# Optimization experiments

Hardware: AMD Instinct MI355X
Metric: run time of the kernel (lower is better)

Reference implementation:

```python
import jax, jax.numpy as jnp
import numpy as np

EPS = 1e-08
NUM_EMBEDDINGS = 8192
EMBEDDING_DIM = 256
N_TOKENS = 32768


def setup_inputs() -> dict:
    key = jax.random.key(0)
    k1, k2, k3 = jax.random.split(key, 3)
    input_data = jax.random.normal(k1, (N_TOKENS, EMBEDDING_DIM), dtype=jnp.float32)
    rand = jax.random.normal(k2, (N_TOKENS, EMBEDDING_DIM), dtype=jnp.float32)
    codebooks = jax.random.normal(k3, (NUM_EMBEDDINGS, EMBEDDING_DIM), dtype=jnp.float32)
    return {"input_data": input_data, "rand": rand, "codebooks": codebooks}


def reference(input_data, rand, codebooks):
    # d2: (N, K) -- this full matrix is what a fused kernel would avoid.
    d2 = (jnp.sum(input_data * input_data, axis=1, keepdims=True)
          - 2.0 * input_data @ codebooks.T
          + jnp.sum(codebooks * codebooks, axis=1)[None, :])
    min_idx = jnp.argmin(d2, axis=1)                      # (N,)
    hard_q = codebooks[min_idx]                           # (N, D)

    # Noise substitution: scale unit-ish gaussian noise to the residual norm.
    r_norm = jnp.linalg.norm(input_data - hard_q, axis=1, keepdims=True)
    n_norm = jnp.linalg.norm(rand, axis=1, keepdims=True)
    quantized_input = input_data + (r_norm / (n_norm + EPS)) * rand

    # Perplexity from codebook usage counts (no grad path in original).
    counts = jnp.zeros((NUM_EMBEDDINGS,), dtype=jnp.float32).at[min_idx].add(1.0)
    total = jnp.maximum(counts.sum(), 1.0)
    avg_probs = counts / total
    perplexity = jnp.exp(-jnp.sum(avg_probs * jnp.log(avg_probs + EPS)))
    num_unique_indices = jnp.sum(counts > 0).astype(jnp.int32)
    return quantized_input, perplexity, num_unique_indices
```

## Files before the change

### kernel.cpp

```cpp
#include <hip/hip_runtime.h>
#include <stdint.h>

#define N_TOKENS 32768
#define N_CODES  8192
#define DIM      256
#define EPSF     1e-8f

typedef __bf16 bf16x8 __attribute__((ext_vector_type(8)));
typedef float  f32x4  __attribute__((ext_vector_type(4)));

#define WS_CNORM_OFF  (4u*1024u*1024u)
#define WS_IDX_OFF    (WS_CNORM_OFF + N_CODES*4u)
#define WS_HIST_OFF   (WS_IDX_OFF + N_TOKENS*4u)

__global__ __launch_bounds__(256) void k_prep(const float* __restrict__ cbf,
                                              unsigned short* __restrict__ cbh,
                                              float* __restrict__ cnorm,
                                              int* __restrict__ hist) {
    const int tid = blockIdx.x * 256 + threadIdx.x;
    if (tid < N_CODES) hist[tid] = 0;

    const int w = threadIdx.x >> 6;
    const int lane = threadIdx.x & 63;
    const int row = blockIdx.x * 4 + w;

    const float4 v = ((const float4*)(cbf + (size_t)row * DIM))[lane];
    float sq = v.x * v.x + v.y * v.y + v.z * v.z + v.w * v.w;

    ushort4 u;
    u.x = __builtin_bit_cast(unsigned short, (__bf16)v.x);
    u.y = __builtin_bit_cast(unsigned short, (__bf16)v.y);
    u.z = __builtin_bit_cast(unsigned short, (__bf16)v.z);
    u.w = __builtin_bit_cast(unsigned short, (__bf16)v.w);
    ((ushort4*)(cbh + (size_t)row * DIM))[lane] = u;

    #pragma unroll
    for (int d = 1; d < 64; d <<= 1) sq += __shfl_xor(sq, d);
    if (lane == 0) cnorm[row] = sq;
}

__global__ __launch_bounds__(256, 1) void k_argmin(const float* __restrict__ X,
                                                   const unsigned short* __restrict__ cbh,
                                                   const float* __restrict__ cnorm,
                                                   int* __restrict__ idxout) {
    __shared__ __attribute__((aligned(16))) char Bs[2][32768];
    __shared__ float redv[4][64];
    __shared__ int   redi[4][64];

    const int tid  = threadIdx.x;
    const int w    = tid >> 6;
    const int lane = tid & 63;
    const int lr   = lane & 15;
    const int lq   = lane >> 4;
    const int r0   = blockIdx.x * 64;
    const int mycol = w * 16 + lr;

    const int half = lane >> 5, l5 = lane & 31;
    int srcoff[8];
    #pragma unroll
    for (int s = 0; s < 8; ++s) {
        const int c = w * 16 + 2 * s + half;
        const int j = (l5 - c) & 31;
        srcoff[s] = c * 512 + j * 16;
    }
    const char* cbb = (const char*)cbh;

    #pragma unroll
    for (int s = 0; s < 8; ++s)
        __builtin_amdgcn_global_load_lds(
            (const __attribute__((address_space(1))) unsigned int*)(cbb + srcoff[s]),
            (__attribute__((address_space(3))) unsigned int*)(&Bs[0][w * 8192 + s * 1024]),
            16, 0, 0);

    bf16x8 A[4][8];
    #pragma unroll
    for (int mf = 0; mf < 4; ++mf) {
        const float* xr = X + (size_t)(r0 + mf * 16 + lr) * DIM;
        #pragma unroll
        for (int kc = 0; kc < 8; ++kc) {
            const float4 a0 = *(const float4*)(xr + kc * 32 + lq * 8);
            const float4 a1 = *(const float4*)(xr + kc * 32 + lq * 8 + 4);
            bf16x8 f;
            f[0] = (__bf16)a0.x; f[1] = (__bf16)a0.y; f[2] = (__bf16)a0.z; f[3] = (__bf16)a0.w;
            f[4] = (__bf16)a1.x; f[5] = (__bf16)a1.y; f[6] = (__bf16)a1.z; f[7] = (__bf16)a1.w;
            A[mf][kc] = f;
        }
    }

    float minv[16];
    int   mini[16];
    #pragma unroll
    for (int i = 0; i < 16; ++i) { minv[i] = 3.4e38f; mini[i] = 0; }

    for (int cc = 0; cc < 128; ++cc) {
        asm volatile("s_waitcnt vmcnt(0)" ::: "memory");

        if (cc + 1 < 128) {
            const char* src = cbb + (size_t)(cc + 1) * 32768;
            char* dst = &Bs[(cc + 1) & 1][w * 8192];
            #pragma unroll
            for (int s = 0; s < 8; ++s)
                __builtin_amdgcn_global_load_lds(
                    (const __attribute__((address_space(1))) unsigned int*)(src + srcoff[s]),
                    (__attribute__((address_space(3))) unsigned int*)(dst + s * 1024),
                    16, 0, 0);
        }

        const float cn = cnorm[cc * 64 + mycol];
        const char* bp = Bs[cc & 1] + mycol * 512;

        f32x4 acc[4];
        #pragma unroll
        for (int mf = 0; mf < 4; ++mf) {
            acc[mf][0] = 0.f; acc[mf][1] = 0.f; acc[mf][2] = 0.f; acc[mf][3] = 0.f;
        }

        #pragma unroll
        for (int kc = 0; kc < 8; ++kc) {
            const bf16x8 b = *(const bf16x8*)(bp + (((kc * 4 + lq + mycol) & 31) << 4));
            #pragma unroll
            for (int mf = 0; mf < 4; ++mf)
                acc[mf] = __builtin_amdgcn_mfma_f32_16x16x32_bf16(A[mf][kc], b, acc[mf], 0, 0, 0);
        }

        const int col = cc * 64 + mycol;
        #pragma unroll
        for (int mf = 0; mf < 4; ++mf)
            #pragma unroll
            for (int r = 0; r < 4; ++r) {
                const float d2 = fmaf(-2.f, acc[mf][r], cn);
                if (d2 < minv[mf * 4 + r]) { minv[mf * 4 + r] = d2; mini[mf * 4 + r] = col; }
            }
    }

    #pragma unroll
    for (int mf = 0; mf < 4; ++mf)
        #pragma unroll
        for (int r = 0; r < 4; ++r) {
            float v = minv[mf * 4 + r]; int ix = mini[mf * 4 + r];
            #pragma unroll
            for (int d = 1; d <= 8; d <<= 1) {
                const float ov = __shfl_xor(v, d);
                const int   oi = __shfl_xor(ix, d);
                if (ov < v || (ov == v && oi < ix)) { v = ov; ix = oi; }
            }
            if (lr == 0) {
                const int row = mf * 16 + lq * 4 + r;
                redv[w][row] = v; redi[w][row] = ix;
            }
        }
    __syncthreads();

    if (tid < 64) {
        float v = redv[0][tid]; int ix = redi[0][tid];
        #pragma unroll
        for (int ww = 1; ww < 4; ++ww) {
            const float ov = redv[ww][tid]; const int oi = redi[ww][tid];
            if (ov < v || (ov == v && oi < ix)) { v = ov; ix = oi; }
        }
        idxout[r0 + tid] = ix;
    }
}

__global__ __launch_bounds__(256) void k_quant(const float* __restrict__ X,
                                               const float* __restrict__ R,
                                               const float* __restrict__ C,
                                               const int* __restrict__ idx,
                                               float* __restrict__ out,
                                               int* __restrict__ hist) {
    const int w = threadIdx.x >> 6;
    const int lane = threadIdx.x & 63;
    const int tok = blockIdx.x * 4 + w;
    const int k = idx[tok];

    const float4 x = ((const float4*)(X + (size_t)tok * DIM))[lane];
    const float4 r = ((const float4*)(R + (size_t)tok * DIM))[lane];
    const float4 c = ((const float4*)(C + (size_t)k * DIM))[lane];

    const float d0 = x.x - c.x, d1 = x.y - c.y, d2 = x.z - c.z, d3 = x.w - c.w;
    float r2 = d0 * d0 + d1 * d1 + d2 * d2 + d3 * d3;
    float n2 = r.x * r.x + r.y * r.y + r.z * r.z + r.w * r.w;
    #pragma unroll
    for (int d = 1; d < 64; d <<= 1) {
        r2 += __shfl_xor(r2, d);
        n2 += __shfl_xor(n2, d);
    }
    const float s = sqrtf(r2) / (sqrtf(n2) + EPSF);

    float4 o;
    o.x = fmaf(s, r.x, x.x);
    o.y = fmaf(s, r.y, x.y);
    o.z = fmaf(s, r.z, x.z);
    o.w = fmaf(s, r.w, x.w);
    ((float4*)(out + (size_t)tok * DIM))[lane] = o;

    if (lane == 0) atomicAdd(&hist[k], 1);
}

__global__ __launch_bounds__(256) void k_stats(const int* __restrict__ hist,
                                               float* __restrict__ outs) {
    float s = 0.f; int u = 0;
    for (int b = threadIdx.x; b < N_CODES; b += 256) {
        const float c = (float)hist[b];
        if (c > 0.f) ++u;
        const float p = c * (1.f / (float)N_TOKENS);
        s += p * logf(p + EPSF);
    }
    #pragma unroll
    for (int d = 1; d < 64; d <<= 1) {
        s += __shfl_xor(s, d);
        u += __shfl_xor(u, d);
    }
    __shared__ float ss[4];
    __shared__ int   su[4];
    const int w = threadIdx.x >> 6, lane = threadIdx.x & 63;
    if (lane == 0) { ss[w] = s; su[w] = u; }
    __syncthreads();
    if (threadIdx.x == 0) {
        const float st = ss[0] + ss[1] + ss[2] + ss[3];
        const int ut = su[0] + su[1] + su[2] + su[3];
        outs[0] = expf(-st);
        outs[1] = (float)ut;
    }
}

extern "C" void kernel_launch(void* const* d_in, const int* in_sizes, int n_in,
                              void* d_out, int out_size, void* d_ws, size_t ws_size,
                              hipStream_t stream) {
    const float* X = (const float*)d_in[0];
    const float* R = (const float*)d_in[1];
    const float* C = (const float*)d_in[2];
    float* out = (float*)d_out;

    char* ws = (char*)d_ws;
    unsigned short* cbh = (unsigned short*)ws;
    float* cnorm = (float*)(ws + WS_CNORM_OFF);
    int*   idx   = (int*)(ws + WS_IDX_OFF);
    int*   hist  = (int*)(ws + WS_HIST_OFF);

    k_prep  <<<N_CODES / 4,  256, 0, stream>>>(C, cbh, cnorm, hist);
    k_argmin<<<N_TOKENS / 64, 256, 0, stream>>>(X, cbh, cnorm, idx);
    k_quant <<<N_TOKENS / 4, 256, 0, stream>>>(X, R, C, idx, out, hist);
    k_stats <<<1, 256, 0, stream>>>(hist, out + (size_t)N_TOKENS * DIM);
}
```

Before: 282.7 us.

## Double token tile per block, stage X via LDS, fold codebook norm into accumulator

Each argmin block now handles 128 tokens instead of 64, so every codebook tile loaded into LDS feeds twice as many MFMAs and the total codebook traffic is halved. X rows are read coalesced, converted to bf16 and staged through a padded LDS region before being loaded into registers. The codebook norm is pre-seeded as -0.5*||c||^2 in the accumulator, and the selection becomes a max on the dot product, which removes the per-element fma. The cnorm load is also prefetched one tile ahead. Register pressure roughly doubles (64 bf16x8 A fragments plus 32 accumulators), which risks spills, and there are now only 256 blocks to spread across the GPU.

```diff
diff --git a/kernel.cpp b/kernel.cpp
--- a/kernel.cpp
+++ b/kernel.cpp
@@ -43,17 +43,39 @@
                                                    const unsigned short* __restrict__ cbh,
                                                    const float* __restrict__ cnorm,
                                                    int* __restrict__ idxout) {
-    __shared__ __attribute__((aligned(16))) char Bs[2][32768];
-    __shared__ float redv[4][64];
-    __shared__ int   redi[4][64];
+    __shared__ __attribute__((aligned(16))) char Bs[2][40960];
+    __shared__ float redv[4][128];
+    __shared__ int   redi[4][128];
 
     const int tid  = threadIdx.x;
     const int w    = tid >> 6;
     const int lane = tid & 63;
     const int lr   = lane & 15;
     const int lq   = lane >> 4;
-    const int r0   = blockIdx.x * 64;
+    const int r0   = blockIdx.x * 128;
     const int mycol = w * 16 + lr;
+
+    {
+        const float4* Xf4 = (const float4*)(X + (size_t)(r0 + 32 * w) * DIM);
+        for (int i = 0; i < 32; ++i) {
+            const float4 v = Xf4[i * 64 + lane];
+            ushort4 u;
+            u.x = __builtin_bit_cast(unsigned short, (__bf16)v.x);
+            u.y = __builtin_bit_cast(unsigned short, (__bf16)v.y);
+            u.z = __builtin_bit_cast(unsigned short, (__bf16)v.z);
+            u.w = __builtin_bit_cast(unsigned short, (__bf16)v.w);
+            *(ushort4*)(&Bs[0][0] + (32 * w + i) * 544 + lane * 8) = u;
+        }
+    }
+    __syncthreads();
+
+    bf16x8 A[8][8];
+    #pragma unroll
+    for (int mf = 0; mf < 8; ++mf)
+        #pragma unroll
+        for (int kc = 0; kc < 8; ++kc)
+            A[mf][kc] = *(const bf16x8*)(&Bs[0][0] + (mf * 16 + lr) * 544 + kc * 64 + lq * 16);
+    __syncthreads();
 
     const int half = lane >> 5, l5 = lane & 31;
     int srcoff[8];
@@ -71,29 +93,16 @@
             (const __attribute__((address_space(1))) unsigned int*)(cbb + srcoff[s]),
             (__attribute__((address_space(3))) unsigned int*)(&Bs[0][w * 8192 + s * 1024]),
             16, 0, 0);
-
-    bf16x8 A[4][8];
-    #pragma unroll
-    for (int mf = 0; mf < 4; ++mf) {
-        const float* xr = X + (size_t)(r0 + mf * 16 + lr) * DIM;
-        #pragma unroll
-        for (int kc = 0; kc < 8; ++kc) {
-            const float4 a0 = *(const float4*)(xr + kc * 32 + lq * 8);
-            const float4 a1 = *(const float4*)(xr + kc * 32 + lq * 8 + 4);
-            bf16x8 f;
-            f[0] = (__bf16)a0.x; f[1] = (__bf16)a0.y; f[2] = (__bf16)a0.z; f[3] = (__bf16)a0.w;
-            f[4] = (__bf16)a1.x; f[5] = (__bf16)a1.y; f[6] = (__bf16)a1.z; f[7] = (__bf16)a1.w;
-            A[mf][kc] = f;
-        }
-    }
-
-    float minv[16];
-    int   mini[16];
-    #pragma unroll
-    for (int i = 0; i < 16; ++i) { minv[i] = 3.4e38f; mini[i] = 0; }
+    float cn_next = cnorm[mycol];
+
+    float maxv[32];
+    int   maxi[32];
+    #pragma unroll
+    for (int i = 0; i < 32; ++i) { maxv[i] = -3.4e38f; maxi[i] = 0; }
 
     for (int cc = 0; cc < 128; ++cc) {
         asm volatile("s_waitcnt vmcnt(0)" ::: "memory");
+        const float cn = cn_next;
 
         if (cc + 1 < 128) {
             const char* src = cbb + (size_t)(cc + 1) * 32768;
@@ -104,45 +113,46 @@
                     (const __attribute__((address_space(1))) unsigned int*)(src + srcoff[s]),
                     (__attribute__((address_space(3))) unsigned int*)(dst + s * 1024),
                     16, 0, 0);
-        }
-
-        const float cn = cnorm[cc * 64 + mycol];
-        const char* bp = Bs[cc & 1] + mycol * 512;
-
-        f32x4 acc[4];
-        #pragma unroll
-        for (int mf = 0; mf < 4; ++mf) {
-            acc[mf][0] = 0.f; acc[mf][1] = 0.f; acc[mf][2] = 0.f; acc[mf][3] = 0.f;
-        }
-
+            cn_next = cnorm[(cc + 1) * 64 + mycol];
+        }
+
+        const float cinit = -0.5f * cn;
+        f32x4 acc[8];
+        #pragma unroll
+        for (int mf = 0; mf < 8; ++mf) {
+            acc[mf][0] = cinit; acc[mf][1] = cinit; acc[mf][2] = cinit; acc[mf][3] = cinit;
+        }
+
+        const char* bp = &Bs[cc & 1][0] + mycol * 512;
         #pragma unroll
         for (int kc = 0; kc < 8; ++kc) {
             const bf16x8 b = *(const bf16x8*)(bp + (((kc * 4 + lq + mycol) & 31) << 4));
             #pragma unroll
-            for (int mf = 0; mf < 4; ++mf)
+            for (int mf = 0; mf < 8; ++mf)
                 acc[mf] = __builtin_amdgcn_mfma_f32_16x16x32_bf16(A[mf][kc], b, acc[mf], 0, 0, 0);
         }
 
         const int col = cc * 64 + mycol;
         #pragma unroll
-        for (int mf = 0; mf < 4; ++mf)
+        for (int mf = 0; mf < 8; ++mf)
             #pragma unroll
             for (int r = 0; r < 4; ++r) {
-                const float d2 = fmaf(-2.f, acc[mf][r], cn);
-                if (d2 < minv[mf * 4 + r]) { minv[mf * 4 + r] = d2; mini[mf * 4 + r] = col; }
+                const float v = acc[mf][r];
+                const int j = mf * 4 + r;
+                if (v > maxv[j]) { maxv[j] = v; maxi[j] = col; }
             }
     }
 
     #pragma unroll
-    for (int mf = 0; mf < 4; ++mf)
+    for (int mf = 0; mf < 8; ++mf)
         #pragma unroll
         for (int r = 0; r < 4; ++r) {
-            float v = minv[mf * 4 + r]; int ix = mini[mf * 4 + r];
+            float v = maxv[mf * 4 + r]; int ix = maxi[mf * 4 + r];
             #pragma unroll
             for (int d = 1; d <= 8; d <<= 1) {
                 const float ov = __shfl_xor(v, d);
                 const int   oi = __shfl_xor(ix, d);
-                if (ov < v || (ov == v && oi < ix)) { v = ov; ix = oi; }
+                if (ov > v || (ov == v && oi < ix)) { v = ov; ix = oi; }
             }
             if (lr == 0) {
                 const int row = mf * 16 + lq * 4 + r;
@@ -151,12 +161,12 @@
         }
     __syncthreads();
 
-    if (tid < 64) {
+    if (tid < 128) {
         float v = redv[0][tid]; int ix = redi[0][tid];
         #pragma unroll
         for (int ww = 1; ww < 4; ++ww) {
             const float ov = redv[ww][tid]; const int oi = redi[ww][tid];
-            if (ov < v || (ov == v && oi < ix)) { v = ov; ix = oi; }
+            if (ov > v || (ov == v && oi < ix)) { v = ov; ix = oi; }
         }
         idxout[r0 + tid] = ix;
     }
@@ -238,8 +248,8 @@
     int*   idx   = (int*)(ws + WS_IDX_OFF);
     int*   hist  = (int*)(ws + WS_HIST_OFF);
 
-    k_prep  <<<N_CODES / 4,  256, 0, stream>>>(C, cbh, cnorm, hist);
-    k_argmin<<<N_TOKENS / 64, 256, 0, stream>>>(X, cbh, cnorm, idx);
-    k_quant <<<N_TOKENS / 4, 256, 0, stream>>>(X, R, C, idx, out, hist);
+    k_prep  <<<N_CODES / 4,   256, 0, stream>>>(C, cbh, cnorm, hist);
+    k_argmin<<<N_TOKENS / 128, 256, 0, stream>>>(X, cbh, cnorm, idx);
+    k_quant <<<N_TOKENS / 4,  256, 0, stream>>>(X, R, C, idx, out, hist);
     k_stats <<<1, 256, 0, stream>>>(hist, out + (size_t)N_TOKENS * DIM);
 }
```

New measurement: 331.9 us. 17.4% more time.
